# Kernel tuning notes

Hardware: AMD Instinct MI355X
Metric: run time of the kernel (lower is better)

## Reference

```python
import jax, jax.numpy as jnp
import numpy as np

# Model dims (see init_kwargs / shape_source)
B = 2048      # batch
CIN = 256     # tabular input features (c_in)
NH = 512      # TabularEncoder hidden width
NENC_HID = 4  # nlayers=6 -> input layer + 4 hidden + output layer
NF = 112      # n_features = num_concepts (conv=False path)
K = 112       # num_concepts
NL = 50       # num_latent_concepts
MC = 100      # num_monte_carlo
NOUT = 200    # num_output


def setup_inputs() -> dict:
    key = jax.random.key(0)
    ks = jax.random.split(key, 8)
    x = jax.random.normal(ks[0], (B, CIN), dtype=jnp.float32)
    enc_Win = jax.random.normal(ks[1], (CIN, NH), dtype=jnp.float32) * (1.0 / np.sqrt(CIN))
    enc_bin = jnp.zeros((NH,), jnp.float32)
    enc_Wh = jax.random.normal(ks[2], (NENC_HID, NH, NH), dtype=jnp.float32) * (1.0 / np.sqrt(NH))
    enc_bh = jnp.zeros((NENC_HID, NH), jnp.float32)
    enc_Wout = jax.random.normal(ks[3], (NH, NF), dtype=jnp.float32) * (1.0 / np.sqrt(NH))
    enc_bout = jnp.zeros((NF,), jnp.float32)
    # Per-concept predictor i has first Linear of shape [NF+i, NL]; pad all to [NF+K, NL]
    # and statically slice rows [:NF+i] in the loop (unused padded rows never touched).
    pred_W1 = jax.random.normal(ks[4], (K, NF + K, NL), dtype=jnp.float32) * (1.0 / np.sqrt(NF))
    pred_b1 = jnp.zeros((K, NL), jnp.float32)
    pred_W2 = jax.random.normal(ks[5], (K, NL), dtype=jnp.float32) * (1.0 / np.sqrt(NL))
    pred_b2 = jnp.zeros((K,), jnp.float32)
    head_W = jax.random.normal(ks[6], (K, NOUT), dtype=jnp.float32) * (1.0 / np.sqrt(K))
    head_b = jnp.zeros((NOUT,), jnp.float32)
    return {
        "x": x,
        "enc_Win": enc_Win, "enc_bin": enc_bin,
        "enc_Wh": enc_Wh, "enc_bh": enc_bh,
        "enc_Wout": enc_Wout, "enc_bout": enc_bout,
        "pred_W1": pred_W1, "pred_b1": pred_b1,
        "pred_W2": pred_W2, "pred_b2": pred_b2,
        "head_W": head_W, "head_b": head_b,
        "epoch": 0,
    }


def reference(x, enc_Win, enc_bin, enc_Wh, enc_bh, enc_Wout, enc_bout,
              pred_W1, pred_b1, pred_W2, pred_b2, head_W, head_b, epoch):
    lrelu = jax.nn.leaky_relu  # negative_slope=0.01, matches nn.LeakyReLU default

    # ---- TabularEncoder (ni=CIN, nhidden=NH, nlayers=6, no=NF) ----
    h = lrelu(x @ enc_Win + enc_bin)
    for i in range(enc_Wh.shape[0]):
        h = lrelu(h @ enc_Wh[i] + enc_bh[i])
    inter = h @ enc_Wout + enc_bout                      # [B, NF]
    Bn = inter.shape[0]

    key = jax.random.key(42)
    c_hard = jnp.zeros((Bn, K, MC), inter.dtype)
    c_probs = []
    for i in range(K):
        W1 = pred_W1[i, :NF + i]                          # [NF+i, NL]
        base = inter @ W1[:NF] + pred_b1[i]               # [B, NL], shared across MC
        if i == 0:
            p1 = jax.nn.sigmoid(lrelu(base) @ pred_W2[i] + pred_b2[i])   # [B]
            p = jnp.broadcast_to(p1[:, None], (Bn, MC))   # expand(-1,-1,MC)
        else:
            # add contribution of the i previously sampled hard concepts, per MC sample
            hpre = base[:, None, :] + jnp.einsum('bim,ih->bmh', c_hard[:, :i], W1[NF:])  # [B,MC,NL]
            p = jax.nn.sigmoid(jnp.einsum('bmh,h->bm', lrelu(hpre), pred_W2[i]) + pred_b2[i])  # [B,MC]
        key, sk = jax.random.split(key)
        samp = jax.random.bernoulli(sk, p).astype(p.dtype)  # torch.bernoulli(concept)
        c_hard = c_hard.at[:, i, :].set(samp)
        c_probs.append(p)

    c_prob = jnp.stack(c_probs, axis=1)                   # [B, K, MC]

    # ---- Head: MC average of softmax probabilities (pred_dim > 1 branch) ----
    logits = jnp.einsum('bkm,ko->bmo', c_hard, head_W) + head_b   # [B, MC, NOUT]
    probs = jax.nn.softmax(logits, axis=-1).mean(axis=1)          # [B, NOUT]
    y_pred_logits = jnp.log(probs + 1e-6)
    return (c_prob, y_pred_logits, c_hard)
```

## Files before the change

kernel.cpp:

```cpp
#include <hip/hip_runtime.h>

typedef unsigned int u32;
typedef unsigned short u16;
typedef unsigned long long u64;

#define YOFF  22937600ull
#define CHOFF 23347200ull

#define OFF_HA    0ull
#define OFF_HB    4194304ull
#define OFF_INTER 8388608ull

__host__ __device__ inline u32 rotl32_(u32 x, int r) { return (x << r) | (x >> (32 - r)); }
__host__ __device__ inline void tf2x32(u32 k0, u32 k1, u32 c0, u32 c1, u32& o0, u32& o1) {
  u32 ks0 = k0, ks1 = k1, ks2 = k0 ^ k1 ^ 0x1BD11BDAu;
  u32 x0 = c0 + ks0, x1 = c1 + ks1;
  const int RA[4] = {13, 15, 26, 6}, RB[4] = {17, 29, 16, 24};
  for (int i = 0; i < 5; ++i) {
    const int* R = (i & 1) ? RB : RA;
    for (int j = 0; j < 4; ++j) { x0 += x1; x1 = rotl32_(x1, R[j]); x1 ^= x0; }
    switch (i) {
      case 0: x0 += ks1; x1 += ks2 + 1u; break;
      case 1: x0 += ks2; x1 += ks0 + 2u; break;
      case 2: x0 += ks0; x1 += ks1 + 3u; break;
      case 3: x0 += ks1; x1 += ks2 + 4u; break;
      case 4: x0 += ks2; x1 += ks0 + 5u; break;
    }
  }
  o0 = x0; o1 = x1;
}

struct SKeys { u32 v[224]; };

template <bool DO_LRELU>
__global__ __launch_bounds__(256) void gemm_bias(const float* __restrict__ A,
                                                 const float* __restrict__ Bm,
                                                 const float* __restrict__ bias,
                                                 float* __restrict__ C,
                                                 int M, int N, int K) {
  __shared__ float As[32][65];
  __shared__ float Bs[32][65];
  const int bm = blockIdx.y * 64, bn = blockIdx.x * 64;
  const int t = threadIdx.x;
  const int ty = t >> 4, tx = t & 15;
  float acc[4][4] = {};
  for (int k0 = 0; k0 < K; k0 += 32) {
#pragma unroll
    for (int l = 0; l < 2; ++l) {
      int e = l * 256 + t;
      int m = e >> 3, k4 = e & 7;
      float4 v = *(const float4*)(A + (size_t)(bm + m) * K + (k0 + k4 * 4));
      As[k4 * 4 + 0][m] = v.x; As[k4 * 4 + 1][m] = v.y;
      As[k4 * 4 + 2][m] = v.z; As[k4 * 4 + 3][m] = v.w;
    }
#pragma unroll
    for (int l = 0; l < 2; ++l) {
      int e = l * 256 + t;
      int k = e >> 4, n4 = e & 15;
      int gn = bn + n4 * 4;
      if (gn < N) {
        float4 v = *(const float4*)(Bm + (size_t)(k0 + k) * N + gn);
        Bs[k][n4 * 4 + 0] = v.x; Bs[k][n4 * 4 + 1] = v.y;
        Bs[k][n4 * 4 + 2] = v.z; Bs[k][n4 * 4 + 3] = v.w;
      } else {
        Bs[k][n4 * 4 + 0] = 0.f; Bs[k][n4 * 4 + 1] = 0.f;
        Bs[k][n4 * 4 + 2] = 0.f; Bs[k][n4 * 4 + 3] = 0.f;
      }
    }
    __syncthreads();
#pragma unroll
    for (int kk = 0; kk < 32; ++kk) {
      float a[4], b[4];
#pragma unroll
      for (int j = 0; j < 4; ++j) { a[j] = As[kk][ty * 4 + j]; b[j] = Bs[kk][tx * 4 + j]; }
#pragma unroll
      for (int i = 0; i < 4; ++i)
#pragma unroll
        for (int j = 0; j < 4; ++j) acc[i][j] = fmaf(a[i], b[j], acc[i][j]);
    }
    __syncthreads();
  }
#pragma unroll
  for (int i = 0; i < 4; ++i) {
#pragma unroll
    for (int j = 0; j < 4; ++j) {
      int m = bm + ty * 4 + i, n = bn + tx * 4 + j;
      if (n < N) {
        float s = acc[i][j] + bias[n];
        if (DO_LRELU) { if (s < 0.f) s = 0.01f * s; }
        C[(size_t)m * N + n] = s;
      }
    }
  }
}

__global__ __launch_bounds__(256) void base_kernel(const float* __restrict__ inter,
                                                   const float* __restrict__ W1,
                                                   const float* __restrict__ pb1,
                                                   float* __restrict__ out) {
  __shared__ float As[112][65];
  __shared__ float Ws[112][64];
  const int i = blockIdx.y;
  const int b0 = blockIdx.x * 64;
  const int t = threadIdx.x;
  const int ty = t >> 4, tx = t & 15;
#pragma unroll
  for (int l = 0; l < 7; ++l) {
    int e4 = l * 256 + t;
    int k4 = e4 % 28, bs = e4 / 28;
    float4 v = *(const float4*)(inter + (size_t)(b0 + bs) * 112 + k4 * 4);
    As[k4 * 4 + 0][bs] = v.x; As[k4 * 4 + 1][bs] = v.y;
    As[k4 * 4 + 2][bs] = v.z; As[k4 * 4 + 3][bs] = v.w;
  }
#pragma unroll
  for (int l = 0; l < 28; ++l) {
    int e = l * 256 + t;
    int r = e >> 6, c = e & 63;
    Ws[r][c] = (c < 50) ? W1[(size_t)i * 11200 + r * 50 + c] : 0.f;
  }
  __syncthreads();
  float acc[4][4] = {};
  for (int kk = 0; kk < 112; ++kk) {
    float a[4], b[4];
#pragma unroll
    for (int j = 0; j < 4; ++j) { a[j] = As[kk][ty * 4 + j]; b[j] = Ws[kk][tx * 4 + j]; }
#pragma unroll
    for (int ii = 0; ii < 4; ++ii)
#pragma unroll
      for (int j = 0; j < 4; ++j) acc[ii][j] = fmaf(a[ii], b[j], acc[ii][j]);
  }
#pragma unroll
  for (int ii = 0; ii < 4; ++ii) {
#pragma unroll
    for (int j = 0; j < 4; ++j) {
      int b = b0 + ty * 4 + ii, h = tx * 4 + j;
      if (h < 50) {
        out[CHOFF + (size_t)b * 11200 + (size_t)i * 100 + h] = acc[ii][j] + pb1[i * 50 + h];
      }
    }
  }
}

__global__ __launch_bounds__(128) void sample_kernel(const float* __restrict__ W1,
                                                     const float* __restrict__ W2,
                                                     const float* __restrict__ b2,
                                                     float* __restrict__ out, SKeys sks) {
  __shared__ __attribute__((aligned(16))) float Wrows[111][52];
  __shared__ float base2[2][52];
  __shared__ float w2row[52];
  const int t = threadIdx.x;
  const int b0 = blockIdx.x * 2, b1 = b0 + 1;
  u64 lo0 = 0, hi0 = 0, lo1 = 0, hi1 = 0;

  for (int i = 0; i < 112; ++i) {
    __syncthreads();
    const float* Wi = W1 + (size_t)i * 11200 + 5600;
    for (int idx = t; idx < i * 50; idx += 128) {
      int r = idx / 50, h = idx - r * 50;
      Wrows[r][h] = Wi[idx];
    }
    if (t < 50) {
      base2[0][t] = out[CHOFF + (size_t)b0 * 11200 + (size_t)i * 100 + t];
      w2row[t]    = W2[i * 50 + t];
    } else if (t < 100) {
      base2[1][t - 50] = out[CHOFF + (size_t)b1 * 11200 + (size_t)i * 100 + (t - 50)];
    }
    __syncthreads();

    if (t < 100) {
      float acc0[52], acc1[52];
#pragma unroll
      for (int h = 0; h < 52; ++h) { acc0[h] = 0.f; acc1[h] = 0.f; }
      for (int r = 0; r < i; ++r) {
        float c0 = (((r < 64) ? (lo0 >> r) : (hi0 >> (r - 64))) & 1ull) ? 1.f : 0.f;
        float c1 = (((r < 64) ? (lo1 >> r) : (hi1 >> (r - 64))) & 1ull) ? 1.f : 0.f;
        const float4* wr = (const float4*)(&Wrows[r][0]);
#pragma unroll
        for (int h4 = 0; h4 < 13; ++h4) {
          float4 w = wr[h4];
          acc0[h4 * 4 + 0] = fmaf(c0, w.x, acc0[h4 * 4 + 0]);
          acc0[h4 * 4 + 1] = fmaf(c0, w.y, acc0[h4 * 4 + 1]);
          acc0[h4 * 4 + 2] = fmaf(c0, w.z, acc0[h4 * 4 + 2]);
          acc0[h4 * 4 + 3] = fmaf(c0, w.w, acc0[h4 * 4 + 3]);
          acc1[h4 * 4 + 0] = fmaf(c1, w.x, acc1[h4 * 4 + 0]);
          acc1[h4 * 4 + 1] = fmaf(c1, w.y, acc1[h4 * 4 + 1]);
          acc1[h4 * 4 + 2] = fmaf(c1, w.z, acc1[h4 * 4 + 2]);
          acc1[h4 * 4 + 3] = fmaf(c1, w.w, acc1[h4 * 4 + 3]);
        }
      }
      float s0 = 0.f, s1 = 0.f;
#pragma unroll
      for (int h = 0; h < 50; ++h) {
        float w2v = w2row[h];
        float v0 = acc0[h] + base2[0][h];
        if (v0 < 0.f) v0 = 0.01f * v0;
        s0 = fmaf(v0, w2v, s0);
        float v1 = acc1[h] + base2[1][h];
        if (v1 < 0.f) v1 = 0.01f * v1;
        s1 = fmaf(v1, w2v, s1);
      }
      float b2v = b2[i];
      float l0 = s0 + b2v, l1 = s1 + b2v;
      float p0 = 1.f / (1.f + expf(-l0));
      float p1 = 1.f / (1.f + expf(-l1));
      u32 sk0 = sks.v[2 * i], sk1 = sks.v[2 * i + 1];
      u32 a0, a1;
      int j0 = b0 * 100 + t, j1 = b1 * 100 + t;
      tf2x32(sk0, sk1, 0u, (u32)j0, a0, a1);
      u32 bits0 = a0 ^ a1;
      u32 fb0 = (bits0 >> 9) | 0x3F800000u;
      float u0; __builtin_memcpy(&u0, &fb0, 4); u0 -= 1.f;
      tf2x32(sk0, sk1, 0u, (u32)j1, a0, a1);
      u32 bits1 = a0 ^ a1;
      u32 fb1 = (bits1 >> 9) | 0x3F800000u;
      float u1; __builtin_memcpy(&u1, &fb1, 4); u1 -= 1.f;
      int smp0 = (u0 < p0) ? 1 : 0;
      int smp1 = (u1 < p1) ? 1 : 0;
      size_t oc0 = (size_t)b0 * 11200 + (size_t)i * 100 + t;
      size_t oc1 = (size_t)b1 * 11200 + (size_t)i * 100 + t;
      out[oc0] = p0;
      out[oc1] = p1;
      out[CHOFF + oc0] = smp0 ? 1.0f : 0.0f;
      out[CHOFF + oc1] = smp1 ? 1.0f : 0.0f;
      if (smp0) { if (i < 64) lo0 |= 1ull << i; else hi0 |= 1ull << (i - 64); }
      if (smp1) { if (i < 64) lo1 |= 1ull << i; else hi1 |= 1ull << (i - 64); }
    }
  }
}

__global__ __launch_bounds__(256) void head_kernel(const float* __restrict__ HW,
                                                   const float* __restrict__ hb,
                                                   float* __restrict__ out) {
  __shared__ unsigned char cS[100][116];
  __shared__ float lgS[50][201];
  const int b = blockIdx.x;
  const int t = threadIdx.x;
  for (int e = t; e < 11200; e += 256) {
    int k = e / 100, m = e - k * 100;
    cS[m][k] = (out[CHOFF + (size_t)b * 11200 + (size_t)k * 100 + m] != 0.f) ? 1 : 0;
  }
  __syncthreads();
  float pacc = 0.f;
  for (int mh = 0; mh < 2; ++mh) {
    for (int l = 0; l < 3; ++l) {
      int tile = l * 256 + t;
      if (tile < 625) {
        int o0 = (tile % 25) * 8;
        int m0 = (tile / 25) * 2;
        float acc[2][8] = {};
        for (int k = 0; k < 112; ++k) {
          float4 wa = *(const float4*)(HW + (size_t)k * 200 + o0);
          float4 wb = *(const float4*)(HW + (size_t)k * 200 + o0 + 4);
          float w[8] = {wa.x, wa.y, wa.z, wa.w, wb.x, wb.y, wb.z, wb.w};
          float c0 = (float)cS[mh * 50 + m0][k];
          float c1 = (float)cS[mh * 50 + m0 + 1][k];
#pragma unroll
          for (int jo = 0; jo < 8; ++jo) {
            acc[0][jo] = fmaf(c0, w[jo], acc[0][jo]);
            acc[1][jo] = fmaf(c1, w[jo], acc[1][jo]);
          }
        }
#pragma unroll
        for (int im = 0; im < 2; ++im)
#pragma unroll
          for (int jo = 0; jo < 8; ++jo) {
            int o = o0 + jo;
            lgS[m0 + im][o] = acc[im][jo] + hb[o];
          }
      }
    }
    __syncthreads();
    if (t < 50) {
      int m = t;
      float mx = -3.0e38f;
      for (int o = 0; o < 200; ++o) mx = fmaxf(mx, lgS[m][o]);
      float s = 0.f;
      for (int o = 0; o < 200; ++o) {
        float e = expf(lgS[m][o] - mx);
        lgS[m][o] = e; s += e;
      }
      float inv = 1.f / s;
      for (int o = 0; o < 200; ++o) lgS[m][o] = lgS[m][o] * inv;
    }
    __syncthreads();
    if (t < 200) { for (int m = 0; m < 50; ++m) pacc += lgS[m][t]; }
    __syncthreads();
  }
  if (t < 200) {
    out[YOFF + (size_t)b * 200 + t] = logf(pacc / 100.f + 1e-6f);
  }
}

extern "C" void kernel_launch(void* const* d_in, const int* in_sizes, int n_in,
                              void* d_out, int out_size, void* d_ws, size_t ws_size,
                              hipStream_t stream) {
  const float* x    = (const float*)d_in[0];
  const float* Win  = (const float*)d_in[1];
  const float* bin  = (const float*)d_in[2];
  const float* Wh   = (const float*)d_in[3];
  const float* bh   = (const float*)d_in[4];
  const float* Wout = (const float*)d_in[5];
  const float* bout = (const float*)d_in[6];
  const float* pW1  = (const float*)d_in[7];
  const float* pb1  = (const float*)d_in[8];
  const float* pW2  = (const float*)d_in[9];
  const float* pb2  = (const float*)d_in[10];
  const float* hW   = (const float*)d_in[11];
  const float* hb   = (const float*)d_in[12];
  float* out = (float*)d_out;
  char* ws = (char*)d_ws;

  float* hA     = (float*)(ws + OFF_HA);
  float* hB     = (float*)(ws + OFF_HB);
  float* interB = (float*)(ws + OFF_INTER);

  gemm_bias<true ><<<dim3(8, 32), 256, 0, stream>>>(x,  Win,             bin,          hA,     2048, 512, 256);
  gemm_bias<true ><<<dim3(8, 32), 256, 0, stream>>>(hA, Wh + 0 * 262144, bh + 0 * 512, hB,     2048, 512, 512);
  gemm_bias<true ><<<dim3(8, 32), 256, 0, stream>>>(hB, Wh + 1 * 262144, bh + 1 * 512, hA,     2048, 512, 512);
  gemm_bias<true ><<<dim3(8, 32), 256, 0, stream>>>(hA, Wh + 2 * 262144, bh + 2 * 512, hB,     2048, 512, 512);
  gemm_bias<true ><<<dim3(8, 32), 256, 0, stream>>>(hB, Wh + 3 * 262144, bh + 3 * 512, hA,     2048, 512, 512);
  gemm_bias<false><<<dim3(2, 32), 256, 0, stream>>>(hA, Wout,            bout,         interB, 2048, 112, 512);

  base_kernel<<<dim3(32, 112), 256, 0, stream>>>(interB, pW1, pb1, out);

  SKeys sks;
  {
    u32 k0 = 0u, k1 = 42u;
    for (int i = 0; i < 112; ++i) {
      u32 nk0, nk1, s0, s1;
      tf2x32(k0, k1, 0u, 0u, nk0, nk1);
      tf2x32(k0, k1, 0u, 1u, s0, s1);
      sks.v[2 * i] = s0; sks.v[2 * i + 1] = s1;
      k0 = nk0; k1 = nk1;
    }
  }
  sample_kernel<<<1024, 128, 0, stream>>>(pW1, pW2, pb2, out, sks);

  head_kernel<<<2048, 256, 0, stream>>>(hW, hb, out);
}
```

Before: 4.185 ms.

## Restructure sampling kernel to one thread per (batch, MC) sample without LDS staging

The sequential concept-sampling kernel now maps each thread to one (batch, MC) pair across 410 blocks of 512 threads, instead of 2 batches per 128-thread block. Weight rows are read directly from global memory (broadcast, cache-friendly) instead of being staged in shared memory with two barriers per concept. Hard samples are written after the loop, since they sit in the same buffer region as the base values the loop still reads. This removes per-iteration syncs and redundant staging and raises occupancy. In exchange, weight loads go through global or scalar caches and each thread keeps a 50-float accumulator array in registers.

```diff
diff --git a/kernel.cpp b/kernel.cpp
--- a/kernel.cpp
+++ b/kernel.cpp
@@ -141,89 +141,53 @@
   }
 }
 
-__global__ __launch_bounds__(128) void sample_kernel(const float* __restrict__ W1,
+__global__ __launch_bounds__(512) void sample_kernel(const float* __restrict__ W1,
                                                      const float* __restrict__ W2,
                                                      const float* __restrict__ b2,
                                                      float* __restrict__ out, SKeys sks) {
-  __shared__ __attribute__((aligned(16))) float Wrows[111][52];
-  __shared__ float base2[2][52];
-  __shared__ float w2row[52];
   const int t = threadIdx.x;
-  const int b0 = blockIdx.x * 2, b1 = b0 + 1;
-  u64 lo0 = 0, hi0 = 0, lo1 = 0, hi1 = 0;
-
-  for (int i = 0; i < 112; ++i) {
-    __syncthreads();
-    const float* Wi = W1 + (size_t)i * 11200 + 5600;
-    for (int idx = t; idx < i * 50; idx += 128) {
-      int r = idx / 50, h = idx - r * 50;
-      Wrows[r][h] = Wi[idx];
-    }
-    if (t < 50) {
-      base2[0][t] = out[CHOFF + (size_t)b0 * 11200 + (size_t)i * 100 + t];
-      w2row[t]    = W2[i * 50 + t];
-    } else if (t < 100) {
-      base2[1][t - 50] = out[CHOFF + (size_t)b1 * 11200 + (size_t)i * 100 + (t - 50)];
-    }
-    __syncthreads();
-
-    if (t < 100) {
-      float acc0[52], acc1[52];
-#pragma unroll
-      for (int h = 0; h < 52; ++h) { acc0[h] = 0.f; acc1[h] = 0.f; }
+  const int p = blockIdx.x * 500 + t;
+  const bool active = (t < 500) && (p < 204800);
+  const int b = p / 100;
+  const int m = p - b * 100;
+  const size_t rowbase = (size_t)b * 11200 + m;
+  const float* __restrict__ baserow = out + CHOFF + (size_t)b * 11200;
+  u64 lo = 0, hi = 0;
+
+  if (active) {
+    for (int i = 0; i < 112; ++i) {
+      const float* __restrict__ Wi = W1 + (size_t)i * 11200 + 5600;
+      float acc[50];
+#pragma unroll
+      for (int h = 0; h < 50; ++h) acc[h] = 0.f;
       for (int r = 0; r < i; ++r) {
-        float c0 = (((r < 64) ? (lo0 >> r) : (hi0 >> (r - 64))) & 1ull) ? 1.f : 0.f;
-        float c1 = (((r < 64) ? (lo1 >> r) : (hi1 >> (r - 64))) & 1ull) ? 1.f : 0.f;
-        const float4* wr = (const float4*)(&Wrows[r][0]);
-#pragma unroll
-        for (int h4 = 0; h4 < 13; ++h4) {
-          float4 w = wr[h4];
-          acc0[h4 * 4 + 0] = fmaf(c0, w.x, acc0[h4 * 4 + 0]);
-          acc0[h4 * 4 + 1] = fmaf(c0, w.y, acc0[h4 * 4 + 1]);
-          acc0[h4 * 4 + 2] = fmaf(c0, w.z, acc0[h4 * 4 + 2]);
-          acc0[h4 * 4 + 3] = fmaf(c0, w.w, acc0[h4 * 4 + 3]);
-          acc1[h4 * 4 + 0] = fmaf(c1, w.x, acc1[h4 * 4 + 0]);
-          acc1[h4 * 4 + 1] = fmaf(c1, w.y, acc1[h4 * 4 + 1]);
-          acc1[h4 * 4 + 2] = fmaf(c1, w.z, acc1[h4 * 4 + 2]);
-          acc1[h4 * 4 + 3] = fmaf(c1, w.w, acc1[h4 * 4 + 3]);
-        }
-      }
-      float s0 = 0.f, s1 = 0.f;
+        float c = (((r < 64) ? (lo >> r) : (hi >> (r - 64))) & 1ull) ? 1.f : 0.f;
+        const float* __restrict__ wr = Wi + r * 50;
+#pragma unroll
+        for (int h = 0; h < 50; ++h) acc[h] = fmaf(c, wr[h], acc[h]);
+      }
+      const float* __restrict__ w2 = W2 + i * 50;
+      const float* bs = baserow + (size_t)i * 100;
+      float s = 0.f;
 #pragma unroll
       for (int h = 0; h < 50; ++h) {
-        float w2v = w2row[h];
-        float v0 = acc0[h] + base2[0][h];
-        if (v0 < 0.f) v0 = 0.01f * v0;
-        s0 = fmaf(v0, w2v, s0);
-        float v1 = acc1[h] + base2[1][h];
-        if (v1 < 0.f) v1 = 0.01f * v1;
-        s1 = fmaf(v1, w2v, s1);
-      }
-      float b2v = b2[i];
-      float l0 = s0 + b2v, l1 = s1 + b2v;
-      float p0 = 1.f / (1.f + expf(-l0));
-      float p1 = 1.f / (1.f + expf(-l1));
-      u32 sk0 = sks.v[2 * i], sk1 = sks.v[2 * i + 1];
+        float v = acc[h] + bs[h];
+        if (v < 0.f) v = 0.01f * v;
+        s = fmaf(v, w2[h], s);
+      }
+      float l = s + b2[i];
+      float pr = 1.f / (1.f + expf(-l));
       u32 a0, a1;
-      int j0 = b0 * 100 + t, j1 = b1 * 100 + t;
-      tf2x32(sk0, sk1, 0u, (u32)j0, a0, a1);
-      u32 bits0 = a0 ^ a1;
-      u32 fb0 = (bits0 >> 9) | 0x3F800000u;
-      float u0; __builtin_memcpy(&u0, &fb0, 4); u0 -= 1.f;
-      tf2x32(sk0, sk1, 0u, (u32)j1, a0, a1);
-      u32 bits1 = a0 ^ a1;
-      u32 fb1 = (bits1 >> 9) | 0x3F800000u;
-      float u1; __builtin_memcpy(&u1, &fb1, 4); u1 -= 1.f;
-      int smp0 = (u0 < p0) ? 1 : 0;
-      int smp1 = (u1 < p1) ? 1 : 0;
-      size_t oc0 = (size_t)b0 * 11200 + (size_t)i * 100 + t;
-      size_t oc1 = (size_t)b1 * 11200 + (size_t)i * 100 + t;
-      out[oc0] = p0;
-      out[oc1] = p1;
-      out[CHOFF + oc0] = smp0 ? 1.0f : 0.0f;
-      out[CHOFF + oc1] = smp1 ? 1.0f : 0.0f;
-      if (smp0) { if (i < 64) lo0 |= 1ull << i; else hi0 |= 1ull << (i - 64); }
-      if (smp1) { if (i < 64) lo1 |= 1ull << i; else hi1 |= 1ull << (i - 64); }
+      tf2x32(sks.v[2 * i], sks.v[2 * i + 1], 0u, (u32)p, a0, a1);
+      u32 fb = ((a0 ^ a1) >> 9) | 0x3F800000u;
+      float u; __builtin_memcpy(&u, &fb, 4); u -= 1.f;
+      int smp = (u < pr) ? 1 : 0;
+      out[rowbase + (size_t)i * 100] = pr;
+      if (smp) { if (i < 64) lo |= 1ull << i; else hi |= 1ull << (i - 64); }
+    }
+    for (int i = 0; i < 112; ++i) {
+      u64 bit = (i < 64) ? (lo >> i) : (hi >> (i - 64));
+      out[CHOFF + rowbase + (size_t)i * 100] = (bit & 1ull) ? 1.0f : 0.0f;
     }
   }
 }
@@ -334,7 +298,7 @@
       k0 = nk0; k1 = nk1;
     }
   }
-  sample_kernel<<<1024, 128, 0, stream>>>(pW1, pW2, pb2, out, sks);
+  sample_kernel<<<410, 512, 0, stream>>>(pW1, pW2, pb2, out, sks);
 
   head_kernel<<<2048, 256, 0, stream>>>(hW, hb, out);
 }
```

After: 3.714 ms. 1.13x faster.
